# Kernel optimization log

Measured on AMD Instinct MI355X. Metric: run time of the kernel, lower is better.

The kernel has to match this reference:

```python
import jax, jax.numpy as jnp
import numpy as np

N = 100000
E = 1600000
IN, HID, OUT = 128, 64, 32


def setup_inputs() -> dict:
    key = jax.random.key(0)
    k1, k2, k3, k4, k5, k6 = jax.random.split(key, 6)
    x = jax.random.normal(k1, (N, IN), dtype=jnp.float32)
    edge_index = jax.random.randint(k2, (2, E), 0, N, dtype=jnp.int64)
    # Glorot-style init for the two GCNConv layers (weight + bias each)
    W1 = jax.random.normal(k3, (IN, HID), dtype=jnp.float32) / np.sqrt(IN)
    b1 = jnp.zeros((HID,), dtype=jnp.float32)
    W2 = jax.random.normal(k4, (HID, OUT), dtype=jnp.float32) / np.sqrt(HID)
    b2 = jnp.zeros((OUT,), dtype=jnp.float32)
    return {"x": x, "edge_index": edge_index, "W1": W1, "b1": b1, "W2": W2, "b2": b2}


def _gcn_norm(edge_index, n, dtype):
    """Add self-loops and compute symmetric normalization coefficients.
    Returns (row, col, norm) where norm[e] = deg[row]^-1/2 * deg[col]^-1/2."""
    loops = jnp.tile(jnp.arange(n, dtype=edge_index.dtype)[None, :], (2, 1))
    ei = jnp.concatenate([edge_index, loops], axis=1)  # [2, E+N]
    row, col = ei[0], ei[1]
    deg = jax.ops.segment_sum(jnp.ones(col.shape, dtype), col, num_segments=n)
    dinv = jnp.where(deg > 0, jax.lax.rsqrt(deg), 0.0)
    norm = dinv[row] * dinv[col]
    return row, col, norm


def _gcn_conv(h, W, b, row, col, norm, n):
    h = h @ W                                   # [N, F_out] dense transform first
    msg = h[row] * norm[:, None]                # gather + edge-normalize
    out = jax.ops.segment_sum(msg, col, num_segments=n)  # scatter-add
    return out + b


def reference(x, edge_index, W1, b1, W2, b2):
    n = x.shape[0]
    row, col, norm = _gcn_norm(edge_index, n, x.dtype)
    h = jax.nn.relu(_gcn_conv(x, W1, b1, row, col, norm, n))
    return _gcn_conv(h, W2, b2, row, col, norm, n)
```

## Files before the change

kernel.cpp:

```cpp
#include <hip/hip_runtime.h>


#define CDIV(a, b) (((a) + (b)-1) / (b))
#define EDGE_TILE 8192
#define BUCKET_CAP 4608

__device__ inline unsigned short f2bf(float f) {
    unsigned int u = __float_as_uint(f);
    u += 0x7FFF + ((u >> 16) & 1);
    return (unsigned short)(u >> 16);
}
__device__ inline void bf2x2(unsigned int u, float& lo, float& hi) {
    lo = __uint_as_float(u << 16);
    hi = __uint_as_float(u & 0xFFFF0000u);
}

__global__ __launch_bounds__(256, 4) void k_sort_gemm1(
    const int* __restrict__ row, const int* __restrict__ col, int e,
    int* __restrict__ gcur, int* __restrict__ bucket,
    const float* __restrict__ x, const float* __restrict__ W,
    unsigned short* __restrict__ hb, int n, int nb_sort) {
    __shared__ float4 smem4[2432];
    int t = threadIdx.x;
    if ((int)blockIdx.x < nb_sort) {
        int* ints   = (int*)smem4;
        int* lstart = ints;
        int* rbase  = ints + 512;
        int* hist   = ints + 1024;
        int* ent    = ints + 1536;
        int base = blockIdx.x * EDGE_TILE;
        int cnt = min(EDGE_TILE, e - base);
        int nbuck = (n + 255) >> 8;
        hist[t] = 0; hist[t + 256] = 0;
        __syncthreads();
        for (int i = t; i < cnt; i += 256) atomicAdd(&hist[col[base + i] >> 8], 1);
        __syncthreads();
        int h0 = hist[2 * t], h1 = hist[2 * t + 1];
        int sum2 = h0 + h1;
        rbase[t] = sum2;
        __syncthreads();
        for (int d = 1; d < 256; d <<= 1) {
            int v = (t >= d) ? rbase[t - d] : 0;
            __syncthreads();
            rbase[t] += v;
            __syncthreads();
        }
        int excl2 = rbase[t] - sum2;
        __syncthreads();
        lstart[2 * t] = excl2;
        lstart[2 * t + 1] = excl2 + h0;
        for (int b = t; b < 512; b += 256) {
            int hbv = hist[b];
            rbase[b] = (hbv > 0) ? atomicAdd(&gcur[b], hbv) : 0;
            hist[b] = 0;
        }
        __syncthreads();
        for (int i = t; i < cnt; i += 256) {
            int c = col[base + i], r = row[base + i];
            int b = c >> 8;
            int rk = atomicAdd(&hist[b], 1);
            ent[lstart[b] + rk] = ((c & 255) << 17) | r;
        }
        __syncthreads();
        for (int i = t; i < cnt; i += 256) {
            int lo = 0, hi = nbuck - 1;
            while (lo < hi) {
                int mid = (lo + hi + 1) >> 1;
                if (lstart[mid] <= i) lo = mid; else hi = mid - 1;
            }
            int b = lo;
            int gi = rbase[b] + (i - lstart[b]);
            if (gi < BUCKET_CAP) bucket[(size_t)b * BUCKET_CAP + gi] = ent[i];
        }
    } else {
        float4* xs = smem4;
        int base = ((int)blockIdx.x - nb_sort) * 64;
        int nodes = min(64, n - base);
        const float4* xg = (const float4*)(x + (size_t)base * 128);
        int lim = nodes * 32;
#pragma unroll
        for (int i = 0; i < 8; ++i) {
            int idx = t + i * 256;
            if (idx < lim) xs[idx] = xg[idx];
        }
        __syncthreads();
        int j = t & 63, g = t >> 6;
        float acc[16];
#pragma unroll
        for (int mm = 0; mm < 16; ++mm) acc[mm] = 0.f;
#pragma unroll 8
        for (int k4 = 0; k4 < 32; ++k4) {
            float w0 = W[(k4 * 4 + 0) * 64 + j];
            float w1 = W[(k4 * 4 + 1) * 64 + j];
            float w2 = W[(k4 * 4 + 2) * 64 + j];
            float w3 = W[(k4 * 4 + 3) * 64 + j];
#pragma unroll
            for (int mm = 0; mm < 16; ++mm) {
                float4 xv = xs[(mm * 4 + g) * 32 + k4];
                acc[mm] = fmaf(xv.x, w0, acc[mm]);
                acc[mm] = fmaf(xv.y, w1, acc[mm]);
                acc[mm] = fmaf(xv.z, w2, acc[mm]);
                acc[mm] = fmaf(xv.w, w3, acc[mm]);
            }
        }
#pragma unroll
        for (int mm = 0; mm < 16; ++mm) {
            int m = base + mm * 4 + g;
            if (m < n) hb[(size_t)m * 64 + j] = f2bf(acc[mm]);
        }
    }
}

__global__ __launch_bounds__(512) void k_bscan(const int* __restrict__ gcur,
                                               int* __restrict__ gbase, int nb) {
    __shared__ int s[512];
    int t = threadIdx.x;
    int v = (t < nb) ? min(gcur[t], BUCKET_CAP) : 0;
    s[t] = v;
    __syncthreads();
    for (int d = 1; d < 512; d <<= 1) {
        int a = (t >= d) ? s[t - d] : 0;
        __syncthreads();
        s[t] += a;
        __syncthreads();
    }
    if (t < nb) gbase[t] = s[t] - v;
}

__global__ __launch_bounds__(256) void k_csr(
    const int* __restrict__ gcur, const int* __restrict__ gbase,
    const int* __restrict__ bucket, int* __restrict__ csr,
    int* __restrict__ start, int* __restrict__ cntg, float* __restrict__ dinv,
    int n) {
    __shared__ int hist[256], lstart[256], lcur[256];
    __shared__ int csrbuf[BUCKET_CAP];
    int b = blockIdx.x, t = threadIdx.x;
    int nodebase = b << 8;
    int nnode = min(256, n - nodebase);
    int m = min(gcur[b], BUCKET_CAP);
    const int* ent = bucket + (size_t)b * BUCKET_CAP;
    hist[t] = 0;
    __syncthreads();
    for (int i = t; i < m; i += 256) atomicAdd(&hist[ent[i] >> 17], 1);
    __syncthreads();
    int v = hist[t];
    lstart[t] = v;
    __syncthreads();
    for (int d = 1; d < 256; d <<= 1) {
        int a = (t >= d) ? lstart[t - d] : 0;
        __syncthreads();
        lstart[t] += a;
        __syncthreads();
    }
    int excl = lstart[t] - v;
    int gb = gbase[b];
    if (t < nnode) {
        int node = nodebase + t;
        start[node] = gb + excl;
        cntg[node] = v;
        dinv[node] = rsqrtf((float)(v + 1));
    }
    __syncthreads();
    lstart[t] = excl;
    lcur[t] = 0;
    __syncthreads();
    for (int i = t; i < m; i += 256) {
        int en = ent[i];
        int local = en >> 17;
        int rk = atomicAdd(&lcur[local], 1);
        csrbuf[lstart[local] + rk] = en & 0x1FFFF;
    }
    __syncthreads();
    for (int i = t; i < m; i += 256) csr[gb + i] = csrbuf[i];
}

__global__ __launch_bounds__(256) void k_agg1(const int* __restrict__ start,
                                              const int* __restrict__ cnt,
                                              const int* __restrict__ csr,
                                              const float* __restrict__ dinv,
                                              const unsigned short* __restrict__ hbm,
                                              const float* __restrict__ b,
                                              const float* __restrict__ W2,
                                              unsigned short* __restrict__ h2b, int n) {
    __shared__ float rowbuf[4][64];
    int node = (blockIdx.x * 256 + threadIdx.x) >> 6;
    int w = threadIdx.x >> 6;
    int lane = threadIdx.x & 63;
    int q = lane >> 3;
    int f4 = lane & 7;
    const int* cs = csr + start[node];
    int d = cnt[node];
    float dc = dinv[node];
    const uint4* hb = (const uint4*)hbm;
    float a0[8], a1[8];
#pragma unroll
    for (int k = 0; k < 8; ++k) { a0[k] = 0.f; a1[k] = 0.f; }
    int j = q;
    for (; j + 8 < d; j += 16) {
        int r0 = cs[j], r1 = cs[j + 8];
        float d0 = dinv[r0], d1 = dinv[r1];
        uint4 v0 = hb[(size_t)r0 * 8 + f4];
        uint4 v1 = hb[(size_t)r1 * 8 + f4];
        float lo, hi;
        bf2x2(v0.x, lo, hi); a0[0] = fmaf(lo, d0, a0[0]); a0[1] = fmaf(hi, d0, a0[1]);
        bf2x2(v0.y, lo, hi); a0[2] = fmaf(lo, d0, a0[2]); a0[3] = fmaf(hi, d0, a0[3]);
        bf2x2(v0.z, lo, hi); a0[4] = fmaf(lo, d0, a0[4]); a0[5] = fmaf(hi, d0, a0[5]);
        bf2x2(v0.w, lo, hi); a0[6] = fmaf(lo, d0, a0[6]); a0[7] = fmaf(hi, d0, a0[7]);
        bf2x2(v1.x, lo, hi); a1[0] = fmaf(lo, d1, a1[0]); a1[1] = fmaf(hi, d1, a1[1]);
        bf2x2(v1.y, lo, hi); a1[2] = fmaf(lo, d1, a1[2]); a1[3] = fmaf(hi, d1, a1[3]);
        bf2x2(v1.z, lo, hi); a1[4] = fmaf(lo, d1, a1[4]); a1[5] = fmaf(hi, d1, a1[5]);
        bf2x2(v1.w, lo, hi); a1[6] = fmaf(lo, d1, a1[6]); a1[7] = fmaf(hi, d1, a1[7]);
    }
    if (j < d) {
        int r = cs[j];
        float d0 = dinv[r];
        uint4 v0 = hb[(size_t)r * 8 + f4];
        float lo, hi;
        bf2x2(v0.x, lo, hi); a0[0] = fmaf(lo, d0, a0[0]); a0[1] = fmaf(hi, d0, a0[1]);
        bf2x2(v0.y, lo, hi); a0[2] = fmaf(lo, d0, a0[2]); a0[3] = fmaf(hi, d0, a0[3]);
        bf2x2(v0.z, lo, hi); a0[4] = fmaf(lo, d0, a0[4]); a0[5] = fmaf(hi, d0, a0[5]);
        bf2x2(v0.w, lo, hi); a0[6] = fmaf(lo, d0, a0[6]); a0[7] = fmaf(hi, d0, a0[7]);
    }
#pragma unroll
    for (int k = 0; k < 8; ++k) a0[k] += a1[k];
#pragma unroll
    for (int k = 0; k < 8; ++k) {
        a0[k] += __shfl_xor(a0[k], 8, 64);
        a0[k] += __shfl_xor(a0[k], 16, 64);
        a0[k] += __shfl_xor(a0[k], 32, 64);
    }
    if (q == 0) {
        uint4 sv = hb[(size_t)node * 8 + f4];
        float s[8], lo, hi;
        bf2x2(sv.x, lo, hi); s[0] = lo; s[1] = hi;
        bf2x2(sv.y, lo, hi); s[2] = lo; s[3] = hi;
        bf2x2(sv.z, lo, hi); s[4] = lo; s[5] = hi;
        bf2x2(sv.w, lo, hi); s[6] = lo; s[7] = hi;
        const float4* b4 = (const float4*)b;
        float4 bv0 = b4[f4 * 2], bv1 = b4[f4 * 2 + 1];
        rowbuf[w][f4 * 8 + 0] = fmaxf(fmaf(s[0], dc, a0[0]) * dc + bv0.x, 0.f);
        rowbuf[w][f4 * 8 + 1] = fmaxf(fmaf(s[1], dc, a0[1]) * dc + bv0.y, 0.f);
        rowbuf[w][f4 * 8 + 2] = fmaxf(fmaf(s[2], dc, a0[2]) * dc + bv0.z, 0.f);
        rowbuf[w][f4 * 8 + 3] = fmaxf(fmaf(s[3], dc, a0[3]) * dc + bv0.w, 0.f);
        rowbuf[w][f4 * 8 + 4] = fmaxf(fmaf(s[4], dc, a0[4]) * dc + bv1.x, 0.f);
        rowbuf[w][f4 * 8 + 5] = fmaxf(fmaf(s[5], dc, a0[5]) * dc + bv1.y, 0.f);
        rowbuf[w][f4 * 8 + 6] = fmaxf(fmaf(s[6], dc, a0[6]) * dc + bv1.z, 0.f);
        rowbuf[w][f4 * 8 + 7] = fmaxf(fmaf(s[7], dc, a0[7]) * dc + bv1.w, 0.f);
    }
    __syncthreads();
    int jj = lane & 31, half = lane >> 5;
    const float* rw = rowbuf[w] + half * 32;
    const float* Wk = W2 + half * 32 * 32 + jj;
    float acc = 0.f;
#pragma unroll 8
    for (int k = 0; k < 32; ++k) acc = fmaf(rw[k], Wk[k * 32], acc);
    acc += __shfl_xor(acc, 32, 64);
    if (half == 0) h2b[(size_t)node * 32 + jj] = f2bf(acc * dc);
}

__global__ __launch_bounds__(256) void k_agg2(const int* __restrict__ start,
                                              const int* __restrict__ cnt,
                                              const int* __restrict__ csr,
                                              const float* __restrict__ dinv,
                                              const unsigned short* __restrict__ hbm,
                                              const float* __restrict__ b,
                                              float* __restrict__ out, int n) {
    int node = (blockIdx.x * 256 + threadIdx.x) >> 6;
    if (node >= n) return;
    int lane = threadIdx.x & 63;
    int q = lane >> 2;
    int f4 = lane & 3;
    const int* cs = csr + start[node];
    int d = cnt[node];
    const uint4* hb = (const uint4*)hbm;
    float a0[8], a1[8];
#pragma unroll
    for (int k = 0; k < 8; ++k) { a0[k] = 0.f; a1[k] = 0.f; }
    int j = q;
    for (; j + 16 < d; j += 32) {
        int r0 = cs[j], r1 = cs[j + 16];
        uint4 v0 = hb[(size_t)r0 * 4 + f4];
        uint4 v1 = hb[(size_t)r1 * 4 + f4];
        float lo, hi;
        bf2x2(v0.x, lo, hi); a0[0] += lo; a0[1] += hi;
        bf2x2(v0.y, lo, hi); a0[2] += lo; a0[3] += hi;
        bf2x2(v0.z, lo, hi); a0[4] += lo; a0[5] += hi;
        bf2x2(v0.w, lo, hi); a0[6] += lo; a0[7] += hi;
        bf2x2(v1.x, lo, hi); a1[0] += lo; a1[1] += hi;
        bf2x2(v1.y, lo, hi); a1[2] += lo; a1[3] += hi;
        bf2x2(v1.z, lo, hi); a1[4] += lo; a1[5] += hi;
        bf2x2(v1.w, lo, hi); a1[6] += lo; a1[7] += hi;
    }
    if (j < d) {
        int r = cs[j];
        uint4 v0 = hb[(size_t)r * 4 + f4];
        float lo, hi;
        bf2x2(v0.x, lo, hi); a0[0] += lo; a0[1] += hi;
        bf2x2(v0.y, lo, hi); a0[2] += lo; a0[3] += hi;
        bf2x2(v0.z, lo, hi); a0[4] += lo; a0[5] += hi;
        bf2x2(v0.w, lo, hi); a0[6] += lo; a0[7] += hi;
    }
#pragma unroll
    for (int k = 0; k < 8; ++k) a0[k] += a1[k];
#pragma unroll
    for (int k = 0; k < 8; ++k) {
        a0[k] += __shfl_xor(a0[k], 4, 64);
        a0[k] += __shfl_xor(a0[k], 8, 64);
        a0[k] += __shfl_xor(a0[k], 16, 64);
        a0[k] += __shfl_xor(a0[k], 32, 64);
    }
    if (q == 0) {
        float dc = dinv[node];
        uint4 sv = hb[(size_t)node * 4 + f4];
        float s[8], lo, hi;
        bf2x2(sv.x, lo, hi); s[0] = lo; s[1] = hi;
        bf2x2(sv.y, lo, hi); s[2] = lo; s[3] = hi;
        bf2x2(sv.z, lo, hi); s[4] = lo; s[5] = hi;
        bf2x2(sv.w, lo, hi); s[6] = lo; s[7] = hi;
        const float4* b4 = (const float4*)b;
        float4 bv0 = b4[f4 * 2], bv1 = b4[f4 * 2 + 1];
        float4 o0, o1;
        o0.x = (a0[0] + s[0]) * dc + bv0.x;
        o0.y = (a0[1] + s[1]) * dc + bv0.y;
        o0.z = (a0[2] + s[2]) * dc + bv0.z;
        o0.w = (a0[3] + s[3]) * dc + bv0.w;
        o1.x = (a0[4] + s[4]) * dc + bv1.x;
        o1.y = (a0[5] + s[5]) * dc + bv1.y;
        o1.z = (a0[6] + s[6]) * dc + bv1.z;
        o1.w = (a0[7] + s[7]) * dc + bv1.w;
        float4* o4 = (float4*)out;
        o4[(size_t)node * 8 + f4 * 2]     = o0;
        o4[(size_t)node * 8 + f4 * 2 + 1] = o1;
    }
}

extern "C" void kernel_launch(void* const* d_in, const int* in_sizes, int n_in,
                              void* d_out, int out_size, void* d_ws, size_t ws_size,
                              hipStream_t stream) {
    const float* x  = (const float*)d_in[0];
    const int*   ei = (const int*)d_in[1];
    const float* W1 = (const float*)d_in[2];
    const float* b1 = (const float*)d_in[3];
    const float* W2 = (const float*)d_in[4];
    const float* b2 = (const float*)d_in[5];
    float* out = (float*)d_out;

    const int n = in_sizes[0] / 128;
    const int e = in_sizes[1] / 2;
    const int* rowp = ei;
    const int* colp = ei + e;

    const int nbuck = CDIV(n, 256);
    const int nb_sort = CDIV(e, EDGE_TILE);
    const int nb_gemm1 = CDIV(n, 64);

    int*   gcur  = (int*)d_ws;
    int*   gbase = gcur + 512;
    int*   start = gbase + 512;
    int*   cnt   = start + n;
    float* dinv  = (float*)(cnt + n);
    int*   csr   = (int*)(dinv + n);
    unsigned short* h1b = (unsigned short*)(csr + e);
    int*   bucket = (int*)(h1b + (size_t)n * 64);
    unsigned short* h2b = (unsigned short*)bucket;

    hipMemsetAsync(gcur, 0, 512 * sizeof(int), stream);

    k_sort_gemm1<<<nb_sort + nb_gemm1, 256, 0, stream>>>(
        rowp, colp, e, gcur, bucket, x, W1, h1b, n, nb_sort);
    k_bscan<<<1, 512, 0, stream>>>(gcur, gbase, nbuck);
    k_csr<<<nbuck, 256, 0, stream>>>(gcur, gbase, bucket, csr, start, cnt, dinv, n);

    k_agg1<<<CDIV(n * 64, 256), 256, 0, stream>>>(start, cnt, csr, dinv, h1b, b1, W2, h2b, n);
    k_agg2<<<CDIV(n * 64, 256), 256, 0, stream>>>(start, cnt, csr, dinv, h2b, b2, out, n);
}
```

Measured before the change: 262.7 us.

## Fold bucket scan into CSR kernel, store bucket ids, halve edge tile

```diff
diff --git a/kernel.cpp b/kernel.cpp
--- a/kernel.cpp
+++ b/kernel.cpp
@@ -2,7 +2,7 @@
 
 
 #define CDIV(a, b) (((a) + (b)-1) / (b))
-#define EDGE_TILE 8192
+#define EDGE_TILE 4096
 #define BUCKET_CAP 4608
 
 __device__ inline unsigned short f2bf(float f) {
@@ -20,17 +20,16 @@
     int* __restrict__ gcur, int* __restrict__ bucket,
     const float* __restrict__ x, const float* __restrict__ W,
     unsigned short* __restrict__ hb, int n, int nb_sort) {
-    __shared__ float4 smem4[2432];
+    __shared__ int smem[8192];
     int t = threadIdx.x;
     if ((int)blockIdx.x < nb_sort) {
-        int* ints   = (int*)smem4;
-        int* lstart = ints;
-        int* rbase  = ints + 512;
-        int* hist   = ints + 1024;
-        int* ent    = ints + 1536;
+        int* lstart = smem;
+        int* rbase  = smem + 512;
+        int* hist   = smem + 1024;
+        int* ent    = smem + 1536;
+        unsigned short* bid = (unsigned short*)(smem + 5632);
         int base = blockIdx.x * EDGE_TILE;
         int cnt = min(EDGE_TILE, e - base);
-        int nbuck = (n + 255) >> 8;
         hist[t] = 0; hist[t + 256] = 0;
         __syncthreads();
         for (int i = t; i < cnt; i += 256) atomicAdd(&hist[col[base + i] >> 8], 1);
@@ -59,21 +58,18 @@
             int c = col[base + i], r = row[base + i];
             int b = c >> 8;
             int rk = atomicAdd(&hist[b], 1);
-            ent[lstart[b] + rk] = ((c & 255) << 17) | r;
+            int p = lstart[b] + rk;
+            ent[p] = ((c & 255) << 17) | r;
+            bid[p] = (unsigned short)b;
         }
         __syncthreads();
         for (int i = t; i < cnt; i += 256) {
-            int lo = 0, hi = nbuck - 1;
-            while (lo < hi) {
-                int mid = (lo + hi + 1) >> 1;
-                if (lstart[mid] <= i) lo = mid; else hi = mid - 1;
-            }
-            int b = lo;
+            int b = bid[i];
             int gi = rbase[b] + (i - lstart[b]);
             if (gi < BUCKET_CAP) bucket[(size_t)b * BUCKET_CAP + gi] = ent[i];
         }
     } else {
-        float4* xs = smem4;
+        float4* xs = (float4*)smem;
         int base = ((int)blockIdx.x - nb_sort) * 64;
         int nodes = min(64, n - base);
         const float4* xg = (const float4*)(x + (size_t)base * 128);
@@ -111,34 +107,36 @@
     }
 }
 
-__global__ __launch_bounds__(512) void k_bscan(const int* __restrict__ gcur,
-                                               int* __restrict__ gbase, int nb) {
-    __shared__ int s[512];
-    int t = threadIdx.x;
-    int v = (t < nb) ? min(gcur[t], BUCKET_CAP) : 0;
-    s[t] = v;
-    __syncthreads();
-    for (int d = 1; d < 512; d <<= 1) {
-        int a = (t >= d) ? s[t - d] : 0;
-        __syncthreads();
-        s[t] += a;
-        __syncthreads();
-    }
-    if (t < nb) gbase[t] = s[t] - v;
-}
-
 __global__ __launch_bounds__(256) void k_csr(
-    const int* __restrict__ gcur, const int* __restrict__ gbase,
-    const int* __restrict__ bucket, int* __restrict__ csr,
-    int* __restrict__ start, int* __restrict__ cntg, float* __restrict__ dinv,
-    int n) {
-    __shared__ int hist[256], lstart[256], lcur[256];
+    const int* __restrict__ gcur, const int* __restrict__ bucket,
+    int* __restrict__ csr, int* __restrict__ start, int* __restrict__ cntg,
+    float* __restrict__ dinv, int n) {
+    __shared__ int hist[256], lstart[256], lcur[256], sc[256];
     __shared__ int csrbuf[BUCKET_CAP];
     int b = blockIdx.x, t = threadIdx.x;
+    int nb = gridDim.x;
+    int* gball = csrbuf;
+    int v0 = (2 * t < nb) ? min(gcur[2 * t], BUCKET_CAP) : 0;
+    int v1 = (2 * t + 1 < nb) ? min(gcur[2 * t + 1], BUCKET_CAP) : 0;
+    int s2 = v0 + v1;
+    sc[t] = s2;
+    __syncthreads();
+    for (int d = 1; d < 256; d <<= 1) {
+        int a = (t >= d) ? sc[t - d] : 0;
+        __syncthreads();
+        sc[t] += a;
+        __syncthreads();
+    }
+    int excl2 = sc[t] - s2;
+    gball[2 * t] = excl2;
+    gball[2 * t + 1] = excl2 + v0;
+    __syncthreads();
+    int gb = gball[b];
     int nodebase = b << 8;
     int nnode = min(256, n - nodebase);
     int m = min(gcur[b], BUCKET_CAP);
     const int* ent = bucket + (size_t)b * BUCKET_CAP;
+    __syncthreads();
     hist[t] = 0;
     __syncthreads();
     for (int i = t; i < m; i += 256) atomicAdd(&hist[ent[i] >> 17], 1);
@@ -153,7 +151,6 @@
         __syncthreads();
     }
     int excl = lstart[t] - v;
-    int gb = gbase[b];
     if (t < nnode) {
         int node = nodebase + t;
         start[node] = gb + excl;
@@ -355,8 +352,7 @@
     const int nb_gemm1 = CDIV(n, 64);
 
     int*   gcur  = (int*)d_ws;
-    int*   gbase = gcur + 512;
-    int*   start = gbase + 512;
+    int*   start = gcur + 512;
     int*   cnt   = start + n;
     float* dinv  = (float*)(cnt + n);
     int*   csr   = (int*)(dinv + n);
@@ -368,8 +364,7 @@
 
     k_sort_gemm1<<<nb_sort + nb_gemm1, 256, 0, stream>>>(
         rowp, colp, e, gcur, bucket, x, W1, h1b, n, nb_sort);
-    k_bscan<<<1, 512, 0, stream>>>(gcur, gbase, nbuck);
-    k_csr<<<nbuck, 256, 0, stream>>>(gcur, gbase, bucket, csr, start, cnt, dinv, n);
+    k_csr<<<nbuck, 256, 0, stream>>>(gcur, bucket, csr, start, cnt, dinv, n);
 
     k_agg1<<<CDIV(n * 64, 256), 256, 0, stream>>>(start, cnt, csr, dinv, h1b, b1, W2, h2b, n);
     k_agg2<<<CDIV(n * 64, 256), 256, 0, stream>>>(start, cnt, csr, dinv, h2b, b2, out, n);
```

Result: slower. 268.0 us (+2.0%).
